# Kernel tuning notes

Measured on AMD Instinct MI355X. Metric: run time of the kernel, lower is better.

Reference implementation:

```python
import jax, jax.numpy as jnp
import numpy as np

EMBED = 1024
HEADS = 16
HEAD_DIM = EMBED // HEADS


def setup_inputs() -> dict:
    key = jax.random.key(0)
    k_x, k_q, k_k, k_v, k_o, k_b = jax.random.split(key, 6)
    s = 1.0 / np.sqrt(EMBED)
    return {
        "x": jax.random.normal(k_x, (4, 2048, EMBED), dtype=jnp.float32),
        "Wq": jax.random.uniform(k_q, (EMBED, EMBED), jnp.float32, -s, s),
        "Wk": jax.random.uniform(k_k, (EMBED, EMBED), jnp.float32, -s, s),
        "Wv": jax.random.uniform(k_v, (EMBED, EMBED), jnp.float32, -s, s),
        "Wo": jax.random.uniform(k_o, (EMBED, EMBED), jnp.float32, -s, s),
        "bo": jax.random.uniform(k_b, (EMBED,), jnp.float32, -s, s),
    }


def reference(x, Wq, Wk, Wv, Wo, bo):
    B, S, E = x.shape
    H, D = HEADS, HEAD_DIM
    # torch nn.Linear: y = x @ W.T
    q = (x @ Wq.T).reshape(B, S, H, D).transpose(0, 2, 1, 3)  # [B,H,S,D]
    k = (x @ Wk.T).reshape(B, S, H, D).transpose(0, 2, 1, 3)
    v = (x @ Wv.T).reshape(B, S, H, D).transpose(0, 2, 1, 3)
    # NOTE: module scales by sqrt(embed_size), not sqrt(head_dim)
    scores = jnp.einsum("bhqd,bhkd->bhqk", q, k) / jnp.sqrt(jnp.float32(E))
    causal = jnp.triu(jnp.ones((S, S), dtype=bool), k=1)
    scores = jnp.where(causal, -jnp.inf, scores)
    attn = jax.nn.softmax(scores, axis=-1)
    out = jnp.einsum("bhqk,bhkd->bhqd", attn, v)  # [B,H,S,D]
    out = out.transpose(0, 2, 1, 3).reshape(B, S, E)
    return out @ Wo.T + bo
```

## Files before the change

### kernel.cpp

```cpp
#include <hip/hip_runtime.h>


#define E_DIM 1024
#define S_LEN 2048
#define BATCH 4
#define NHEAD 16
#define HDIM  64

using short8 = __attribute__((ext_vector_type(8))) short;
using f32x4  = __attribute__((ext_vector_type(4))) float;

__device__ inline unsigned short f2bf(float f) {
    unsigned int u = __builtin_bit_cast(unsigned int, f);
    u += 0x7FFFu + ((u >> 16) & 1u);
    return (unsigned short)(u >> 16);
}

__global__ __launch_bounds__(256) void cvt_f32_bf16(
        const float* __restrict__ src, unsigned short* __restrict__ dst, int n) {
    int i = (blockIdx.x * 256 + threadIdx.x) * 4;
    if (i >= n) return;
    float4 v = *reinterpret_cast<const float4*>(src + i);
    ushort4 o;
    o.x = f2bf(v.x); o.y = f2bf(v.y); o.z = f2bf(v.z); o.w = f2bf(v.w);
    *reinterpret_cast<ushort4*>(dst + i) = o;
}

__global__ __launch_bounds__(256) void gemm_qkv(
        const unsigned short* __restrict__ xb,
        const unsigned short* __restrict__ wb,
        unsigned short* __restrict__ qkv) {
    const int z = blockIdx.z;
    const unsigned short* Bw = wb + (size_t)z * (E_DIM * E_DIM);
    unsigned short* Out = qkv + (size_t)z * ((size_t)BATCH * NHEAD * S_LEN * HDIM);
    const int m0 = blockIdx.x * 128, n0 = blockIdx.y * 128;
    const int tid = threadIdx.x;
    const int lane = tid & 63, w = tid >> 6;
    const int wm = w >> 1, wn = w & 1;
    const int col = lane & 15, hi = lane >> 4;

    __shared__ __align__(16) unsigned short Alds[128 * 40];
    __shared__ __align__(16) unsigned short Blds[128 * 40];

    f32x4 acc[4][4] = {};

    for (int kt = 0; kt < E_DIM / 32; ++kt) {
        const int k0 = kt * 32;
#pragma unroll
        for (int i = 0; i < 2; ++i) {
            int c = tid + i * 256;
            int r = c >> 2, c8 = (c & 3) * 8;
            short8 va = *reinterpret_cast<const short8*>(xb + (size_t)(m0 + r) * E_DIM + k0 + c8);
            short8 vb = *reinterpret_cast<const short8*>(Bw + (size_t)(n0 + r) * E_DIM + k0 + c8);
            *reinterpret_cast<short8*>(&Alds[r * 40 + c8]) = va;
            *reinterpret_cast<short8*>(&Blds[r * 40 + c8]) = vb;
        }
        __syncthreads();
        short8 af[4], bf[4];
#pragma unroll
        for (int mt = 0; mt < 4; ++mt)
            af[mt] = *reinterpret_cast<const short8*>(&Alds[(wm * 64 + mt * 16 + col) * 40 + hi * 8]);
#pragma unroll
        for (int nt = 0; nt < 4; ++nt)
            bf[nt] = *reinterpret_cast<const short8*>(&Blds[(wn * 64 + nt * 16 + col) * 40 + hi * 8]);
#pragma unroll
        for (int mt = 0; mt < 4; ++mt)
#pragma unroll
            for (int nt = 0; nt < 4; ++nt)
                acc[mt][nt] = __builtin_amdgcn_mfma_f32_16x16x32_bf16(af[mt], bf[nt], acc[mt][nt], 0, 0, 0);
        __syncthreads();
    }

    const float scale = (z == 0) ? (0.03125f * 1.44269504f) : 1.0f;
#pragma unroll
    for (int mt = 0; mt < 4; ++mt) {
#pragma unroll
        for (int nt = 0; nt < 4; ++nt) {
#pragma unroll
            for (int b = 0; b < 4; ++b) {
                int m = m0 + wm * 64 + mt * 16 + hi * 4 + b;
                int n = n0 + wn * 64 + nt * 16 + col;
                int bidx = m >> 11, s = m & 2047;
                int h = n >> 6, d = n & 63;
                size_t off = (((size_t)(bidx * NHEAD + h)) * S_LEN + s) * HDIM + d;
                Out[off] = f2bf(acc[mt][nt][b] * scale);
            }
        }
    }
}

__global__ __launch_bounds__(512, 4) void attn_fwd(
        const unsigned short* __restrict__ Q,
        const unsigned short* __restrict__ K,
        const unsigned short* __restrict__ V,
        unsigned short* __restrict__ Out) {
    const int g = blockIdx.x;
    const int p = g >> 6;
    const int bh = (g & 7) + ((g >> 3) & 7) * 8;
    const int b_idx = bh >> 4, h = bh & 15;
    const int tid = threadIdx.x, lane = tid & 63, w = tid >> 6;
    const int col = lane & 15, hi = lane >> 4;

    const unsigned short* Qb = Q + (size_t)bh * (S_LEN * HDIM);
    const unsigned short* Kb = K + (size_t)bh * (S_LEN * HDIM);
    const unsigned short* Vb = V + (size_t)bh * (S_LEN * HDIM);

    __shared__ __align__(16) unsigned short Klds[64 * 64];
    __shared__ __align__(16) unsigned short Vt[64 * 64];
    __shared__ __align__(16) unsigned short Plds[8][16 * 64];
    unsigned short* Pl = &Plds[w][0];

    const int kr = tid >> 3, kc8 = (tid & 7) * 8;
    const int ksw = kc8 ^ ((kr & 7) << 3);
    const int vr = tid & 63, vc8 = (tid >> 6) * 8;

#pragma unroll
    for (int pass = 0; pass < 2; ++pass) {
        const int qt = pass ? (15 - p) : p;
        const int nt = 2 * qt + 2;
        const int q0 = qt * 128 + w * 16;

        short8 qf0, qf1;
        {
            const unsigned short* qrow = Qb + (size_t)(q0 + col) * HDIM;
            qf0 = *reinterpret_cast<const short8*>(qrow + hi * 8);
            qf1 = *reinterpret_cast<const short8*>(qrow + 32 + hi * 8);
        }

        f32x4 acc[4] = {};
        float mrun[4], lrun[4];
#pragma unroll
        for (int b = 0; b < 4; ++b) { mrun[b] = -INFINITY; lrun[b] = 0.f; }

        short8 pk = *reinterpret_cast<const short8*>(Kb + (size_t)kr * HDIM + kc8);
        short8 pv = *reinterpret_cast<const short8*>(Vb + (size_t)vr * HDIM + vc8);

        for (int t = 0; t < nt; ++t) {
            const int kv0 = t * 64;
            __syncthreads();
            *reinterpret_cast<short8*>(&Klds[kr * 64 + ksw]) = pk;
#pragma unroll
            for (int j = 0; j < 8; ++j) {
                const int d0 = vc8 + j;
                Vt[d0 * 64 + (vr ^ ((d0 & 7) << 3))] = (unsigned short)pv[j];
            }
            if (t < nt - 1) {
                const int kn = kv0 + 64;
                pk = *reinterpret_cast<const short8*>(Kb + (size_t)(kn + kr) * HDIM + kc8);
                pv = *reinterpret_cast<const short8*>(Vb + (size_t)(kn + vr) * HDIM + vc8);
            }
            __syncthreads();

            if (kv0 <= q0 + 15) {
                f32x4 s[4];
                __builtin_amdgcn_s_setprio(1);
#pragma unroll
                for (int kc = 0; kc < 4; ++kc) {
                    const int row = kc * 16 + col;
                    const int sw = (row & 7) << 3;
                    const unsigned short* kb = Klds + row * 64;
                    short8 kf0 = *reinterpret_cast<const short8*>(kb + ((hi * 8) ^ sw));
                    short8 kf1 = *reinterpret_cast<const short8*>(kb + ((32 + hi * 8) ^ sw));
                    f32x4 z4 = {0.f, 0.f, 0.f, 0.f};
                    z4 = __builtin_amdgcn_mfma_f32_16x16x32_bf16(qf0, kf0, z4, 0, 0, 0);
                    s[kc] = __builtin_amdgcn_mfma_f32_16x16x32_bf16(qf1, kf1, z4, 0, 0, 0);
                }
                __builtin_amdgcn_s_setprio(0);

                if (kv0 + 63 > q0) {
#pragma unroll
                    for (int kc = 0; kc < 4; ++kc) {
                        int kg = kv0 + kc * 16 + col;
#pragma unroll
                        for (int b = 0; b < 4; ++b) {
                            int qg = q0 + hi * 4 + b;
                            if (kg > qg) s[kc][b] = -INFINITY;
                        }
                    }
                }

                float vb[4];
#pragma unroll
                for (int b = 0; b < 4; ++b) {
                    float v = fmaxf(fmaxf(s[0][b], s[1][b]), fmaxf(s[2][b], s[3][b]));
                    v = fmaxf(v, __shfl_xor(v, 1));
                    v = fmaxf(v, __shfl_xor(v, 2));
                    v = fmaxf(v, __shfl_xor(v, 4));
                    v = fmaxf(v, __shfl_xor(v, 8));
                    vb[b] = v;
                }
                bool grow = (vb[0] > mrun[0] + 11.5f) || (vb[1] > mrun[1] + 11.5f) ||
                            (vb[2] > mrun[2] + 11.5f) || (vb[3] > mrun[3] + 11.5f);
                if (__any(grow)) {
#pragma unroll
                    for (int b = 0; b < 4; ++b) {
                        float mnew = fmaxf(mrun[b], vb[b]);
                        float fac = exp2f(mrun[b] - mnew);
                        mrun[b] = mnew;
                        lrun[b] *= fac;
#pragma unroll
                        for (int dt = 0; dt < 4; ++dt) acc[dt][b] *= fac;
                    }
                }
#pragma unroll
                for (int kc = 0; kc < 4; ++kc) {
                    const int c = kc * 16 + col;
#pragma unroll
                    for (int b = 0; b < 4; ++b) {
                        float pp = exp2f(s[kc][b] - mrun[b]);
                        lrun[b] += pp;
                        const int r = hi * 4 + b;
                        Pl[r * 64 + (c ^ ((r & 7) << 3))] = f2bf(pp);
                    }
                }
                const int psw = (col & 7) << 3;
                short8 pf0 = *reinterpret_cast<const short8*>(Pl + col * 64 + ((hi * 8) ^ psw));
                short8 pf1 = *reinterpret_cast<const short8*>(Pl + col * 64 + ((32 + hi * 8) ^ psw));

                __builtin_amdgcn_s_setprio(1);
#pragma unroll
                for (int dt = 0; dt < 4; ++dt) {
                    const int row = dt * 16 + col;
                    const int sw = (row & 7) << 3;
                    const unsigned short* vbp = Vt + row * 64;
                    short8 vf0 = *reinterpret_cast<const short8*>(vbp + ((hi * 8) ^ sw));
                    short8 vf1 = *reinterpret_cast<const short8*>(vbp + ((32 + hi * 8) ^ sw));
                    acc[dt] = __builtin_amdgcn_mfma_f32_16x16x32_bf16(pf0, vf0, acc[dt], 0, 0, 0);
                    acc[dt] = __builtin_amdgcn_mfma_f32_16x16x32_bf16(pf1, vf1, acc[dt], 0, 0, 0);
                }
                __builtin_amdgcn_s_setprio(0);
            }
        }

#pragma unroll
        for (int b = 0; b < 4; ++b) {
            float l = lrun[b];
            l += __shfl_xor(l, 1);
            l += __shfl_xor(l, 2);
            l += __shfl_xor(l, 4);
            l += __shfl_xor(l, 8);
            float inv = 1.0f / l;
            int qg = q0 + hi * 4 + b;
#pragma unroll
            for (int dt = 0; dt < 4; ++dt) {
                size_t off = ((size_t)(b_idx * S_LEN + qg)) * E_DIM + h * HDIM + dt * 16 + col;
                Out[off] = f2bf(acc[dt][b] * inv);
            }
        }
    }
}

__global__ __launch_bounds__(256) void gemm_out(
        const unsigned short* __restrict__ Ab,
        const unsigned short* __restrict__ Bw,
        const float* __restrict__ bias,
        float* __restrict__ Out) {
    const int m0 = blockIdx.x * 128, n0 = blockIdx.y * 128;
    const int tid = threadIdx.x;
    const int lane = tid & 63, w = tid >> 6;
    const int wm = w >> 1, wn = w & 1;
    const int col = lane & 15, hi = lane >> 4;

    __shared__ __align__(16) unsigned short Alds[128 * 40];
    __shared__ __align__(16) unsigned short Blds[128 * 40];

    f32x4 acc[4][4] = {};

    for (int kt = 0; kt < E_DIM / 32; ++kt) {
        const int k0 = kt * 32;
#pragma unroll
        for (int i = 0; i < 2; ++i) {
            int c = tid + i * 256;
            int r = c >> 2, c8 = (c & 3) * 8;
            short8 va = *reinterpret_cast<const short8*>(Ab + (size_t)(m0 + r) * E_DIM + k0 + c8);
            short8 vb = *reinterpret_cast<const short8*>(Bw + (size_t)(n0 + r) * E_DIM + k0 + c8);
            *reinterpret_cast<short8*>(&Alds[r * 40 + c8]) = va;
            *reinterpret_cast<short8*>(&Blds[r * 40 + c8]) = vb;
        }
        __syncthreads();
        short8 af[4], bf[4];
#pragma unroll
        for (int mt = 0; mt < 4; ++mt)
            af[mt] = *reinterpret_cast<const short8*>(&Alds[(wm * 64 + mt * 16 + col) * 40 + hi * 8]);
#pragma unroll
        for (int nt = 0; nt < 4; ++nt)
            bf[nt] = *reinterpret_cast<const short8*>(&Blds[(wn * 64 + nt * 16 + col) * 40 + hi * 8]);
#pragma unroll
        for (int mt = 0; mt < 4; ++mt)
#pragma unroll
            for (int nt = 0; nt < 4; ++nt)
                acc[mt][nt] = __builtin_amdgcn_mfma_f32_16x16x32_bf16(af[mt], bf[nt], acc[mt][nt], 0, 0, 0);
        __syncthreads();
    }

#pragma unroll
    for (int mt = 0; mt < 4; ++mt) {
#pragma unroll
        for (int nt = 0; nt < 4; ++nt) {
#pragma unroll
            for (int b = 0; b < 4; ++b) {
                int m = m0 + wm * 64 + mt * 16 + hi * 4 + b;
                int n = n0 + wn * 64 + nt * 16 + col;
                Out[(size_t)m * E_DIM + n] = acc[mt][nt][b] + bias[n];
            }
        }
    }
}

extern "C" void kernel_launch(void* const* d_in, const int* in_sizes, int n_in,
                              void* d_out, int out_size, void* d_ws, size_t ws_size,
                              hipStream_t stream) {
    const float* x  = (const float*)d_in[0];
    const float* Wq = (const float*)d_in[1];
    const float* Wk = (const float*)d_in[2];
    const float* Wv = (const float*)d_in[3];
    const float* Wo = (const float*)d_in[4];
    const float* bo = (const float*)d_in[5];
    float* out = (float*)d_out;

    unsigned short* ws   = (unsigned short*)d_ws;
    unsigned short* xb   = ws;
    unsigned short* wb   = xb + (size_t)8192 * 1024;
    unsigned short* qkv  = wb + (size_t)4 * 1024 * 1024;
    unsigned short* attn = qkv + (size_t)3 * 8192 * 1024;

    cvt_f32_bf16<<<8192, 256, 0, stream>>>(x, xb, 8192 * 1024);
    cvt_f32_bf16<<<1024, 256, 0, stream>>>(Wq, wb, 1024 * 1024);
    cvt_f32_bf16<<<1024, 256, 0, stream>>>(Wk, wb + 1048576, 1024 * 1024);
    cvt_f32_bf16<<<1024, 256, 0, stream>>>(Wv, wb + 2 * 1048576, 1024 * 1024);
    cvt_f32_bf16<<<1024, 256, 0, stream>>>(Wo, wb + 3 * 1048576, 1024 * 1024);

    gemm_qkv<<<dim3(64, 8, 3), 256, 0, stream>>>(xb, wb, qkv);
    attn_fwd<<<512, 512, 0, stream>>>(qkv, qkv + 8388608, qkv + 2 * 8388608, attn);
    gemm_out<<<dim3(64, 8), 256, 0, stream>>>(attn, wb + 3 * 1048576, bo, out);
}
```

Measured before the change: 218.6 us.

## Use direct global-to-LDS loads in GEMMs and merge conversion kernels

The register-staged global-to-LDS copies in both projection GEMMs are replaced with direct global_load_lds 16-byte loads, and the LDS row stride drops from 40 to 32 shorts so the layout matches the per-wave contiguous writes. The five fp32-to-bf16 conversion launches are merged into one kernel to cut launch overhead. The unpadded 32-short stride may add LDS bank conflicts on the fragment reads, and there is still no double buffering, so the loads are not overlapped with compute.

After: 196.5 us. 1.11x faster.

```diff
diff --git a/kernel.cpp b/kernel.cpp
--- a/kernel.cpp
+++ b/kernel.cpp
@@ -10,16 +10,33 @@
 using short8 = __attribute__((ext_vector_type(8))) short;
 using f32x4  = __attribute__((ext_vector_type(4))) float;
 
+#define GLD16(gp, lp) __builtin_amdgcn_global_load_lds( \
+    (const __attribute__((address_space(1))) void*)(gp), \
+    (__attribute__((address_space(3))) void*)(lp), 16, 0, 0)
+
 __device__ inline unsigned short f2bf(float f) {
     unsigned int u = __builtin_bit_cast(unsigned int, f);
     u += 0x7FFFu + ((u >> 16) & 1u);
     return (unsigned short)(u >> 16);
 }
 
-__global__ __launch_bounds__(256) void cvt_f32_bf16(
-        const float* __restrict__ src, unsigned short* __restrict__ dst, int n) {
-    int i = (blockIdx.x * 256 + threadIdx.x) * 4;
-    if (i >= n) return;
+__global__ __launch_bounds__(256) void cvt_all(
+        const float* __restrict__ x,  const float* __restrict__ wq,
+        const float* __restrict__ wk, const float* __restrict__ wv,
+        const float* __restrict__ wo,
+        unsigned short* __restrict__ xb, unsigned short* __restrict__ wb) {
+    const int bid = blockIdx.x;
+    const float* src;
+    unsigned short* dst;
+    int blk;
+    if (bid < 8192) { src = x; dst = xb; blk = bid; }
+    else {
+        const int wsel = (bid - 8192) >> 10;
+        blk = (bid - 8192) & 1023;
+        src = (wsel == 0) ? wq : (wsel == 1) ? wk : (wsel == 2) ? wv : wo;
+        dst = wb + (size_t)wsel * 1048576;
+    }
+    const int i = (blk * 256 + threadIdx.x) * 4;
     float4 v = *reinterpret_cast<const float4*>(src + i);
     ushort4 o;
     o.x = f2bf(v.x); o.y = f2bf(v.y); o.z = f2bf(v.z); o.w = f2bf(v.w);
@@ -39,30 +56,29 @@
     const int wm = w >> 1, wn = w & 1;
     const int col = lane & 15, hi = lane >> 4;
 
-    __shared__ __align__(16) unsigned short Alds[128 * 40];
-    __shared__ __align__(16) unsigned short Blds[128 * 40];
+    __shared__ __align__(16) unsigned short Alds[128 * 32];
+    __shared__ __align__(16) unsigned short Blds[128 * 32];
+
+    const int srow = tid >> 2;
+    const int sc8  = (tid & 3) * 8;
+    const int wofs = w * 512;
 
     f32x4 acc[4][4] = {};
 
     for (int kt = 0; kt < E_DIM / 32; ++kt) {
         const int k0 = kt * 32;
-#pragma unroll
-        for (int i = 0; i < 2; ++i) {
-            int c = tid + i * 256;
-            int r = c >> 2, c8 = (c & 3) * 8;
-            short8 va = *reinterpret_cast<const short8*>(xb + (size_t)(m0 + r) * E_DIM + k0 + c8);
-            short8 vb = *reinterpret_cast<const short8*>(Bw + (size_t)(n0 + r) * E_DIM + k0 + c8);
-            *reinterpret_cast<short8*>(&Alds[r * 40 + c8]) = va;
-            *reinterpret_cast<short8*>(&Blds[r * 40 + c8]) = vb;
-        }
+        GLD16(xb + (size_t)(m0 + srow) * E_DIM + k0 + sc8,       &Alds[wofs]);
+        GLD16(xb + (size_t)(m0 + 64 + srow) * E_DIM + k0 + sc8,  &Alds[2048 + wofs]);
+        GLD16(Bw + (size_t)(n0 + srow) * E_DIM + k0 + sc8,       &Blds[wofs]);
+        GLD16(Bw + (size_t)(n0 + 64 + srow) * E_DIM + k0 + sc8,  &Blds[2048 + wofs]);
         __syncthreads();
         short8 af[4], bf[4];
 #pragma unroll
         for (int mt = 0; mt < 4; ++mt)
-            af[mt] = *reinterpret_cast<const short8*>(&Alds[(wm * 64 + mt * 16 + col) * 40 + hi * 8]);
+            af[mt] = *reinterpret_cast<const short8*>(&Alds[(wm * 64 + mt * 16 + col) * 32 + hi * 8]);
 #pragma unroll
         for (int nt = 0; nt < 4; ++nt)
-            bf[nt] = *reinterpret_cast<const short8*>(&Blds[(wn * 64 + nt * 16 + col) * 40 + hi * 8]);
+            bf[nt] = *reinterpret_cast<const short8*>(&Blds[(wn * 64 + nt * 16 + col) * 32 + hi * 8]);
 #pragma unroll
         for (int mt = 0; mt < 4; ++mt)
 #pragma unroll
@@ -261,30 +277,29 @@
     const int wm = w >> 1, wn = w & 1;
     const int col = lane & 15, hi = lane >> 4;
 
-    __shared__ __align__(16) unsigned short Alds[128 * 40];
-    __shared__ __align__(16) unsigned short Blds[128 * 40];
+    __shared__ __align__(16) unsigned short Alds[128 * 32];
+    __shared__ __align__(16) unsigned short Blds[128 * 32];
+
+    const int srow = tid >> 2;
+    const int sc8  = (tid & 3) * 8;
+    const int wofs = w * 512;
 
     f32x4 acc[4][4] = {};
 
     for (int kt = 0; kt < E_DIM / 32; ++kt) {
         const int k0 = kt * 32;
-#pragma unroll
-        for (int i = 0; i < 2; ++i) {
-            int c = tid + i * 256;
-            int r = c >> 2, c8 = (c & 3) * 8;
-            short8 va = *reinterpret_cast<const short8*>(Ab + (size_t)(m0 + r) * E_DIM + k0 + c8);
-            short8 vb = *reinterpret_cast<const short8*>(Bw + (size_t)(n0 + r) * E_DIM + k0 + c8);
-            *reinterpret_cast<short8*>(&Alds[r * 40 + c8]) = va;
-            *reinterpret_cast<short8*>(&Blds[r * 40 + c8]) = vb;
-        }
+        GLD16(Ab + (size_t)(m0 + srow) * E_DIM + k0 + sc8,       &Alds[wofs]);
+        GLD16(Ab + (size_t)(m0 + 64 + srow) * E_DIM + k0 + sc8,  &Alds[2048 + wofs]);
+        GLD16(Bw + (size_t)(n0 + srow) * E_DIM + k0 + sc8,       &Blds[wofs]);
+        GLD16(Bw + (size_t)(n0 + 64 + srow) * E_DIM + k0 + sc8,  &Blds[2048 + wofs]);
         __syncthreads();
         short8 af[4], bf[4];
 #pragma unroll
         for (int mt = 0; mt < 4; ++mt)
-            af[mt] = *reinterpret_cast<const short8*>(&Alds[(wm * 64 + mt * 16 + col) * 40 + hi * 8]);
+            af[mt] = *reinterpret_cast<const short8*>(&Alds[(wm * 64 + mt * 16 + col) * 32 + hi * 8]);
 #pragma unroll
         for (int nt = 0; nt < 4; ++nt)
-            bf[nt] = *reinterpret_cast<const short8*>(&Blds[(wn * 64 + nt * 16 + col) * 40 + hi * 8]);
+            bf[nt] = *reinterpret_cast<const short8*>(&Blds[(wn * 64 + nt * 16 + col) * 32 + hi * 8]);
 #pragma unroll
         for (int mt = 0; mt < 4; ++mt)
 #pragma unroll
@@ -324,12 +339,7 @@
     unsigned short* qkv  = wb + (size_t)4 * 1024 * 1024;
     unsigned short* attn = qkv + (size_t)3 * 8192 * 1024;
 
-    cvt_f32_bf16<<<8192, 256, 0, stream>>>(x, xb, 8192 * 1024);
-    cvt_f32_bf16<<<1024, 256, 0, stream>>>(Wq, wb, 1024 * 1024);
-    cvt_f32_bf16<<<1024, 256, 0, stream>>>(Wk, wb + 1048576, 1024 * 1024);
-    cvt_f32_bf16<<<1024, 256, 0, stream>>>(Wv, wb + 2 * 1048576, 1024 * 1024);
-    cvt_f32_bf16<<<1024, 256, 0, stream>>>(Wo, wb + 3 * 1048576, 1024 * 1024);
-
+    cvt_all<<<12288, 256, 0, stream>>>(x, Wq, Wk, Wv, Wo, xb, wb);
     gemm_qkv<<<dim3(64, 8, 3), 256, 0, stream>>>(xb, wb, qkv);
     attn_fwd<<<512, 512, 0, stream>>>(qkv, qkv + 8388608, qkv + 2 * 8388608, attn);
     gemm_out<<<dim3(64, 8), 256, 0, stream>>>(attn, wb + 3 * 1048576, bo, out);
```
